# Kernel tuning notes

Hardware: AMD Instinct MI355X
Metric: run time of the kernel (lower is better)

## Reference

```python
import jax, jax.numpy as jnp
import numpy as np

# dims per init_kwargs
B, T, N = 2, 16, 8192
F0, F1, F2 = 4, 8, 8
K = 3
D0, D1 = 8, 4


def setup_inputs() -> dict:
    ks = jax.random.split(jax.random.key(0), 11)
    x = jax.random.normal(ks[0], (B, T, F0, N), jnp.float32)
    # GSO: random symmetric-ish shift operator, scaled for spectral stability
    S = jax.random.normal(ks[1], (N, N), jnp.float32) / np.float32(np.sqrt(N))
    h1 = jax.random.normal(ks[2], (F1, K, F0), jnp.float32) * 0.1   # layer-1 filter taps
    b1 = jax.random.normal(ks[3], (F1, 1), jnp.float32) * 0.1
    h2 = jax.random.normal(ks[4], (F2, K, F1), jnp.float32) * 0.1   # layer-2 filter taps
    b2 = jax.random.normal(ks[5], (F2, 1), jnp.float32) * 0.1
    W1 = jax.random.normal(ks[6], (D0, F2), jnp.float32) * 0.1      # readout Linear 1
    bw1 = jax.random.normal(ks[7], (D0,), jnp.float32) * 0.1
    W2 = jax.random.normal(ks[8], (D1, D0), jnp.float32) * 0.1      # readout Linear 2
    bw2 = jax.random.normal(ks[9], (D1,), jnp.float32) * 0.1
    return {"x": x, "S": S, "h1": h1, "b1": b1, "h2": h2, "b2": b2,
            "W1": W1, "bw1": bw1, "W2": W2, "bw2": bw2}


def graph_filter(x, S, h, b):
    # x: [B,T,Fin,N]; h: [Fout,K,Fin]; b: [Fout,1]
    # z_k = z_{k-1} @ S  (diffusion over node dim, LSIGF with E=1, no delay)
    taps = [x]
    for _ in range(h.shape[1] - 1):
        taps.append(jnp.matmul(taps[-1], S))
    z = jnp.stack(taps, axis=2)                       # [B,T,K,Fin,N]
    return jnp.einsum('gkf,btkfn->btgn', h, z) + b    # [B,T,Fout,N]


def reference(x, S, h1, b1, h2, b2, W1, bw1, W2, bw2):
    y = jnp.tanh(graph_filter(x, S, h1, b1))          # [B,T,F1,N]
    y = jnp.tanh(graph_filter(y, S, h2, b2))          # [B,T,F2,N]
    # per-node readout: Linear over feature axis
    y = jnp.swapaxes(y, 2, 3)                         # [B,T,N,F2]
    y = jnp.tanh(jnp.einsum('btnf,df->btnd', y, W1) + bw1)
    y = jnp.einsum('btnd,ed->btne', y, W2) + bw2
    return jnp.swapaxes(y, 2, 3)                      # [B,T,D1,N]
```

## Files before the change

### kernel.cpp

```cpp
#include <hip/hip_runtime.h>
#include <math.h>

constexpr int NN = 8192;

typedef short bh8 __attribute__((ext_vector_type(8)));
typedef float fl4 __attribute__((ext_vector_type(4)));

__device__ __forceinline__ float bf2f(ushort h) {
  return __uint_as_float(((uint)h) << 16);
}
__device__ __forceinline__ ushort f2bf(float f) {
  uint u = __float_as_uint(f);
  return (ushort)((u + 0x7fffu + ((u >> 16) & 1u)) >> 16);
}

constexpr size_t OFF_P  = 16;
constexpr size_t OFF_XC = 4096;
constexpr size_t OFF_Z1 = OFF_XC + 2097152;
constexpr size_t OFF_Y1 = OFF_Z1 + 2097152;
constexpr size_t OFF_V1 = OFF_Y1 + 4194304;
constexpr size_t OFF_ST = 33554432;
constexpr size_t OFF_CF = 167772160;

constexpr int PO_H1 = 0, PO_B1 = 96, PO_H2 = 104, PO_B2 = 296;
constexpr int PO_W1 = 304, PO_BW1 = 368, PO_W2 = 376, PO_BW2 = 408;

__global__ __launch_bounds__(256) void detect_convert(
    const ushort* __restrict__ Sraw,
    const void* h1, const void* b1, const void* h2, const void* b2,
    const void* W1, const void* bw1, const void* W2, const void* bw2,
    char* __restrict__ ws) {
  __shared__ int smax[256];
  __shared__ int sflag;
  const int t = threadIdx.x;
  int mx = 0;
  for (int k = 0; k < 32; ++k) {
    ushort u = Sraw[(size_t)(t * 32 + k) * 2];
    int e = (u >> 7) & 0xff;
    mx = mx > e ? mx : e;
  }
  smax[t] = mx;
  __syncthreads();
  for (int s = 128; s > 0; s >>= 1) {
    if (t < s) smax[t] = smax[t] > smax[t + s] ? smax[t] : smax[t + s];
    __syncthreads();
  }
  if (t == 0) {
    sflag = (smax[0] >= 0x90) ? 1 : 0;
    *(int*)ws = sflag;
  }
  __syncthreads();
  const int f32 = sflag;
  float* pb = (float*)(ws + OFF_P);
  const void* ptrs[8] = {h1, b1, h2, b2, W1, bw1, W2, bw2};
  const int offs[8] = {PO_H1, PO_B1, PO_H2, PO_B2, PO_W1, PO_BW1, PO_W2, PO_BW2};
  const int lens[8] = {96, 8, 192, 8, 64, 8, 32, 4};
  for (int idx = t; idx < 412; idx += 256) {
#pragma unroll
    for (int s = 0; s < 8; ++s) {
      if (idx >= offs[s] && idx < offs[s] + lens[s]) {
        const int j = idx - offs[s];
        pb[idx] = f32 ? ((const float*)ptrs[s])[j]
                      : bf2f(((const ushort*)ptrs[s])[j]);
      }
    }
  }
}

__global__ __launch_bounds__(256) void convert_x(const void* __restrict__ xraw,
                                                 const char* __restrict__ wsro,
                                                 ushort* __restrict__ xc) {
  const int f32 = *(const int*)wsro;
  const int i = (blockIdx.x * 256 + threadIdx.x) * 4;
  if (f32) {
    float4 v = *(const float4*)((const float*)xraw + i);
    uint2 o;
    o.x = (uint)f2bf(v.x) | ((uint)f2bf(v.y) << 16);
    o.y = (uint)f2bf(v.z) | ((uint)f2bf(v.w) << 16);
    *(uint2*)&xc[i] = o;
  } else {
    *(uint2*)&xc[i] = *(const uint2*)((const ushort*)xraw + i);
  }
}

template <int Z>
__global__ __launch_bounds__(256) void reduce_cvt(const float* __restrict__ src,
                                                  size_t slice,
                                                  ushort* __restrict__ dst) {
  const size_t i = (size_t)(blockIdx.x * 256 + threadIdx.x) * 4;
  float4 s = *(const float4*)&src[i];
#pragma unroll
  for (int z = 1; z < Z; ++z) {
    float4 t = *(const float4*)&src[(size_t)z * slice + i];
    s.x += t.x; s.y += t.y; s.z += t.z; s.w += t.w;
  }
  uint2 o;
  o.x = (uint)f2bf(s.x) | ((uint)f2bf(s.y) << 16);
  o.y = (uint)f2bf(s.z) | ((uint)f2bf(s.w) << 16);
  *(uint2*)&dst[i] = o;
}

__global__ __launch_bounds__(256) void transpose_k(const ushort* __restrict__ Sraw,
                                                   const char* __restrict__ wsro,
                                                   ushort* __restrict__ St) {
  __shared__ uint tileU[64][33];
  const int f32 = *(const int*)wsro;
  const int t = threadIdx.x;
  const int tn = blockIdx.x * 64;
  const int tk = blockIdx.y * 64;
  {
    const int kp = t >> 3;
    const int c  = (t & 7) * 8;
    if (f32) {
      const float* r0 = (const float*)Sraw + (size_t)(tk + 2 * kp) * NN + tn + c;
      float4 a0 = *(const float4*)r0;
      float4 a1 = *(const float4*)(r0 + 4);
      float4 b0 = *(const float4*)(r0 + NN);
      float4 b1 = *(const float4*)(r0 + NN + 4);
      tileU[c + 0][kp] = (uint)f2bf(a0.x) | ((uint)f2bf(b0.x) << 16);
      tileU[c + 1][kp] = (uint)f2bf(a0.y) | ((uint)f2bf(b0.y) << 16);
      tileU[c + 2][kp] = (uint)f2bf(a0.z) | ((uint)f2bf(b0.z) << 16);
      tileU[c + 3][kp] = (uint)f2bf(a0.w) | ((uint)f2bf(b0.w) << 16);
      tileU[c + 4][kp] = (uint)f2bf(a1.x) | ((uint)f2bf(b1.x) << 16);
      tileU[c + 5][kp] = (uint)f2bf(a1.y) | ((uint)f2bf(b1.y) << 16);
      tileU[c + 6][kp] = (uint)f2bf(a1.z) | ((uint)f2bf(b1.z) << 16);
      tileU[c + 7][kp] = (uint)f2bf(a1.w) | ((uint)f2bf(b1.w) << 16);
    } else {
      const ushort* r0 = Sraw + (size_t)(tk + 2 * kp) * NN + tn + c;
      uint4 ua = *(const uint4*)r0;
      uint4 ub = *(const uint4*)(r0 + NN);
      const ushort* ap = (const ushort*)&ua;
      const ushort* bp = (const ushort*)&ub;
#pragma unroll
      for (int j = 0; j < 8; ++j)
        tileU[c + j][kp] = (uint)ap[j] | ((uint)bp[j] << 16);
    }
  }
  __syncthreads();
  {
    const int n = t >> 2;
#pragma unroll
    for (int it = 0; it < 2; ++it) {
      const int q = (t & 3) + 4 * it;
      uint4 w;
      w.x = tileU[n][q * 4 + 0];
      w.y = tileU[n][q * 4 + 1];
      w.z = tileU[n][q * 4 + 2];
      w.w = tileU[n][q * 4 + 3];
      *(uint4*)&St[(size_t)(tn + n) * NN + tk + q * 8] = w;
    }
  }
}

template <int KR>
__global__ __launch_bounds__(256, 2) void gemm_t(const ushort* __restrict__ A,
                                                 const ushort* __restrict__ St,
                                                 float* __restrict__ CF) {
  __shared__ ushort As[2][128 * 64];
  __shared__ ushort Bs[2][128 * 64];
  const int tid = threadIdx.x;
  const int wave = tid >> 6, lane = tid & 63;
  const int lrow = lane & 15, quad = lane >> 4;
  const int m0 = blockIdx.y * 128;
  const int n0 = blockIdx.x * 128;
  const int kc0 = blockIdx.z * KR;
  const int wm = (wave & 1) * 64;
  const int wn = (wave >> 1) * 64;
  float* CP = CF + (size_t)blockIdx.z * (size_t)(gridDim.y * 128) * NN;

  const ushort* ap[4];
  const ushort* bp[4];
#pragma unroll
  for (int r = 0; r < 4; ++r) {
    const int s = r * 256 + tid;
    const int row = s >> 3, g = (s & 7) ^ (row & 7);
    ap[r] = A + (size_t)(m0 + row) * NN + g * 8;
    bp[r] = St + (size_t)(n0 + row) * NN + g * 8;
  }

  fl4 acc[4][4];
#pragma unroll
  for (int i = 0; i < 4; ++i)
#pragma unroll
    for (int j = 0; j < 4; ++j) acc[i][j] = (fl4){0.f, 0.f, 0.f, 0.f};

#define STAGE(buf, kc)                                                         \
  {                                                                            \
    _Pragma("unroll")                                                          \
    for (int r = 0; r < 4; ++r) {                                              \
      __builtin_amdgcn_global_load_lds(                                        \
          (__attribute__((address_space(1))) void*)(ap[r] + (kc)),             \
          (__attribute__((address_space(3))) void*)                            \
              &As[buf][(r * 256 + wave * 64) * 8],                             \
          16, 0, 0);                                                           \
      __builtin_amdgcn_global_load_lds(                                        \
          (__attribute__((address_space(1))) void*)(bp[r] + (kc)),             \
          (__attribute__((address_space(3))) void*)                            \
              &Bs[buf][(r * 256 + wave * 64) * 8],                             \
          16, 0, 0);                                                           \
    }                                                                          \
  }

#define COMPUTE(buf)                                                           \
  {                                                                            \
    _Pragma("unroll")                                                          \
    for (int is = 0; is < 2; ++is) {                                           \
      bh8 af[4], bf[4];                                                        \
      const int G = is * 4 + quad;                                             \
      _Pragma("unroll")                                                        \
      for (int i = 0; i < 4; ++i) {                                            \
        const int row = wm + i * 16 + lrow;                                    \
        af[i] = *(const bh8*)&As[buf][row * 64 + ((G ^ (row & 7)) * 8)];       \
      }                                                                        \
      _Pragma("unroll")                                                        \
      for (int j = 0; j < 4; ++j) {                                            \
        const int row = wn + j * 16 + lrow;                                    \
        bf[j] = *(const bh8*)&Bs[buf][row * 64 + ((G ^ (row & 7)) * 8)];       \
      }                                                                        \
      _Pragma("unroll")                                                        \
      for (int i = 0; i < 4; ++i)                                              \
        _Pragma("unroll")                                                      \
        for (int j = 0; j < 4; ++j)                                            \
          acc[i][j] = __builtin_amdgcn_mfma_f32_16x16x32_bf16(af[i], bf[j],    \
                                                              acc[i][j], 0, 0, 0); \
    }                                                                          \
  }

#define BARRIER()                                                              \
  {                                                                            \
    asm volatile("" ::: "memory");                                             \
    __builtin_amdgcn_s_barrier();                                              \
    asm volatile("" ::: "memory");                                             \
  }

  STAGE(0, kc0)
  STAGE(1, kc0 + 64)
  const int kend = kc0 + KR;
#pragma unroll 1
  for (int kc = kc0; kc < kend; kc += 128) {
    asm volatile("s_waitcnt vmcnt(8)" ::: "memory");
    BARRIER()
    COMPUTE(0)
    asm volatile("s_waitcnt lgkmcnt(0)" ::: "memory");
    BARRIER()
    if (kc + 128 < kend) {
      STAGE(0, kc + 128)
      asm volatile("s_waitcnt vmcnt(8)" ::: "memory");
    } else {
      asm volatile("s_waitcnt vmcnt(0)" ::: "memory");
    }
    BARRIER()
    COMPUTE(1)
    if (kc + 192 < kend) {
      asm volatile("s_waitcnt lgkmcnt(0)" ::: "memory");
      BARRIER()
      STAGE(1, kc + 192)
    }
  }
#undef STAGE
#undef COMPUTE
#undef BARRIER

#pragma unroll
  for (int i = 0; i < 4; ++i)
#pragma unroll
    for (int j = 0; j < 4; ++j)
#pragma unroll
      for (int rr = 0; rr < 4; ++rr) {
        const int row = m0 + wm + i * 16 + quad * 4 + rr;
        const int col = n0 + wn + j * 16 + lrow;
        CP[(size_t)row * NN + col] = acc[i][j][rr];
      }
}

__global__ __launch_bounds__(256) void combine1(const ushort* __restrict__ xc,
                                                const ushort* __restrict__ z1,
                                                const float* __restrict__ z2f,
                                                const char* __restrict__ wsro,
                                                ushort* __restrict__ y1) {
  const float* pb = (const float*)(wsro + OFF_P);
  __shared__ float hs[96], bs[8];
  const int t = threadIdx.x;
  if (t < 96) hs[t] = pb[PO_H1 + t];
  if (t < 8) bs[t] = pb[PO_B1 + t];
  __syncthreads();
  const int idx = blockIdx.x * 256 + t;
  const int bt = idx >> 11;
  const int n4 = (idx & 2047) * 4;
  float acc[8][4];
#pragma unroll
  for (int g = 0; g < 8; ++g)
#pragma unroll
    for (int v = 0; v < 4; ++v) acc[g][v] = bs[g];
#pragma unroll
  for (int k = 0; k < 3; ++k)
#pragma unroll
    for (int f = 0; f < 4; ++f) {
      const size_t off = (size_t)(bt * 4 + f) * NN + n4;
      float val[4];
      if (k == 2) {
        float4 w = *(const float4*)&z2f[off];
#pragma unroll
        for (int z = 1; z < 8; ++z) {
          float4 u = *(const float4*)&z2f[(size_t)z * 1048576 + off];
          w.x += u.x; w.y += u.y; w.z += u.z; w.w += u.w;
        }
        val[0] = w.x; val[1] = w.y; val[2] = w.z; val[3] = w.w;
      } else {
        const ushort* pp = (k == 0) ? xc : z1;
        uint2 w = *(const uint2*)&pp[off];
        val[0] = bf2f(w.x & 0xffff); val[1] = bf2f(w.x >> 16);
        val[2] = bf2f(w.y & 0xffff); val[3] = bf2f(w.y >> 16);
      }
#pragma unroll
      for (int g = 0; g < 8; ++g) {
        const float hw = hs[(g * 3 + k) * 4 + f];
#pragma unroll
        for (int v = 0; v < 4; ++v) acc[g][v] += hw * val[v];
      }
    }
#pragma unroll
  for (int g = 0; g < 8; ++g) {
    ushort o[4];
#pragma unroll
    for (int v = 0; v < 4; ++v) o[v] = f2bf(tanhf(acc[g][v]));
    uint2 w;
    w.x = (uint)o[0] | ((uint)o[1] << 16);
    w.y = (uint)o[2] | ((uint)o[3] << 16);
    *(uint2*)&y1[(size_t)(bt * 8 + g) * NN + n4] = w;
  }
}

__global__ __launch_bounds__(256) void combine2(const ushort* __restrict__ y1,
                                                const ushort* __restrict__ v1,
                                                const float* __restrict__ v2f,
                                                const char* __restrict__ wsro,
                                                void* __restrict__ outv) {
  const float* pb = (const float*)(wsro + OFF_P);
  const int f32 = *(const int*)wsro;
  __shared__ float h2s[192], W1s[64], W2s[32], b2s[8], bw1s[8], bw2s[4];
  const int t = threadIdx.x;
  if (t < 192) h2s[t] = pb[PO_H2 + t];
  if (t < 64) W1s[t] = pb[PO_W1 + t];
  if (t < 32) W2s[t] = pb[PO_W2 + t];
  if (t < 8) { b2s[t] = pb[PO_B2 + t]; bw1s[t] = pb[PO_BW1 + t]; }
  if (t < 4) bw2s[t] = pb[PO_BW2 + t];
  __syncthreads();
  const int idx = blockIdx.x * 256 + t;
  const int bt = idx >> 12;
  const int n2 = (idx & 4095) * 2;
  float acc[8][2];
#pragma unroll
  for (int g = 0; g < 8; ++g) { acc[g][0] = b2s[g]; acc[g][1] = b2s[g]; }
#pragma unroll
  for (int k = 0; k < 3; ++k)
#pragma unroll
    for (int g1 = 0; g1 < 8; ++g1) {
      const size_t off = (size_t)(bt * 8 + g1) * NN + n2;
      float v0, v1v;
      if (k == 2) {
        float2 w = *(const float2*)&v2f[off];
#pragma unroll
        for (int z = 1; z < 4; ++z) {
          float2 u = *(const float2*)&v2f[(size_t)z * 2097152 + off];
          w.x += u.x; w.y += u.y;
        }
        v0 = w.x; v1v = w.y;
      } else {
        const ushort* pp = (k == 0) ? y1 : v1;
        uint w = *(const uint*)&pp[off];
        v0 = bf2f(w & 0xffff); v1v = bf2f(w >> 16);
      }
#pragma unroll
      for (int g2 = 0; g2 < 8; ++g2) {
        const float hw = h2s[(g2 * 3 + k) * 8 + g1];
        acc[g2][0] += hw * v0;
        acc[g2][1] += hw * v1v;
      }
    }
#pragma unroll
  for (int g = 0; g < 8; ++g) {
    acc[g][0] = tanhf(acc[g][0]);
    acc[g][1] = tanhf(acc[g][1]);
  }
  float o[4][2];
#pragma unroll
  for (int e = 0; e < 4; ++e) { o[e][0] = bw2s[e]; o[e][1] = bw2s[e]; }
#pragma unroll
  for (int d = 0; d < 8; ++d) {
    float s0 = bw1s[d], s1 = bw1s[d];
#pragma unroll
    for (int f = 0; f < 8; ++f) {
      const float w = W1s[d * 8 + f];
      s0 += w * acc[f][0];
      s1 += w * acc[f][1];
    }
    s0 = tanhf(s0);
    s1 = tanhf(s1);
#pragma unroll
    for (int e = 0; e < 4; ++e) {
      const float w = W2s[e * 8 + d];
      o[e][0] += w * s0;
      o[e][1] += w * s1;
    }
  }
#pragma unroll
  for (int e = 0; e < 4; ++e) {
    const size_t off = (size_t)(bt * 4 + e) * NN + n2;
    if (f32) {
      float2 w = {o[e][0], o[e][1]};
      *(float2*)&((float*)outv)[off] = w;
    } else {
      uint w = (uint)f2bf(o[e][0]) | ((uint)f2bf(o[e][1]) << 16);
      *(uint*)&((ushort*)outv)[off] = w;
    }
  }
}

extern "C" void kernel_launch(void* const* d_in, const int* in_sizes, int n_in,
                              void* d_out, int out_size, void* d_ws,
                              size_t ws_size, hipStream_t stream) {
  (void)in_sizes; (void)n_in; (void)out_size; (void)ws_size;
  const void* x = d_in[0];
  const ushort* S = (const ushort*)d_in[1];
  char* ws = (char*)d_ws;
  ushort* xc = (ushort*)(ws + OFF_XC);
  ushort* z1 = (ushort*)(ws + OFF_Z1);
  ushort* y1 = (ushort*)(ws + OFF_Y1);
  ushort* v1 = (ushort*)(ws + OFF_V1);
  float* CF = (float*)(ws + OFF_CF);
  ushort* St = (ushort*)(ws + OFF_ST);

  detect_convert<<<1, 256, 0, stream>>>(S, d_in[2], d_in[3], d_in[4], d_in[5],
                                        d_in[6], d_in[7], d_in[8], d_in[9], ws);
  convert_x<<<1024, 256, 0, stream>>>(x, ws, xc);
  transpose_k<<<dim3(128, 128), 256, 0, stream>>>(S, ws, St);

  gemm_t<1024><<<dim3(64, 1, 8), 256, 0, stream>>>(xc, St, CF);
  reduce_cvt<8><<<1024, 256, 0, stream>>>(CF, (size_t)1048576, z1);

  gemm_t<1024><<<dim3(64, 1, 8), 256, 0, stream>>>(z1, St, CF);
  combine1<<<256, 256, 0, stream>>>(xc, z1, CF, ws, y1);

  gemm_t<2048><<<dim3(64, 2, 4), 256, 0, stream>>>(y1, St, CF);
  reduce_cvt<4><<<2048, 256, 0, stream>>>(CF, (size_t)2097152, v1);

  gemm_t<2048><<<dim3(64, 2, 4), 256, 0, stream>>>(v1, St, CF);
  combine2<<<512, 256, 0, stream>>>(y1, v1, CF, ws, (void*)d_out);
}
```

Measured before the change: 591.3 us.

## Fuse all stages into one persistent kernel with software grid barriers

Replaces the sequence of ten kernel launches (convert, transpose, four split-K GEMMs, reductions and combines) with a single persistent kernel of 512 blocks that runs every stage in order, separated by atomic-counter grid barriers. This is meant to remove launch gaps and kernel-boundary drains between the short stages. The cost is that the transpose is now a grid-stride loop over fewer blocks, and progress depends on all 512 blocks being co-resident (two per CU), with a spin barrier that has a timeout guard and could silently break synchronisation.

```diff
diff --git a/kernel.cpp b/kernel.cpp
--- a/kernel.cpp
+++ b/kernel.cpp
@@ -2,6 +2,7 @@
 #include <math.h>
 
 constexpr int NN = 8192;
+constexpr int NBLK = 512;
 
 typedef short bh8 __attribute__((ext_vector_type(8)));
 typedef float fl4 __attribute__((ext_vector_type(4)));
@@ -14,18 +15,19 @@
   return (ushort)((u + 0x7fffu + ((u >> 16) & 1u)) >> 16);
 }
 
-constexpr size_t OFF_P  = 16;
-constexpr size_t OFF_XC = 4096;
-constexpr size_t OFF_Z1 = OFF_XC + 2097152;
-constexpr size_t OFF_Y1 = OFF_Z1 + 2097152;
-constexpr size_t OFF_V1 = OFF_Y1 + 4194304;
-constexpr size_t OFF_ST = 33554432;
-constexpr size_t OFF_CF = 167772160;
+constexpr size_t OFF_P   = 16;
+constexpr size_t OFF_BAR = 2048;
+constexpr size_t OFF_XC  = 4096;
+constexpr size_t OFF_Z1  = OFF_XC + 2097152;
+constexpr size_t OFF_Y1  = OFF_Z1 + 2097152;
+constexpr size_t OFF_V1  = OFF_Y1 + 4194304;
+constexpr size_t OFF_ST  = 33554432;
+constexpr size_t OFF_CF  = 167772160;
 
 constexpr int PO_H1 = 0, PO_B1 = 96, PO_H2 = 104, PO_B2 = 296;
 constexpr int PO_W1 = 304, PO_BW1 = 368, PO_W2 = 376, PO_BW2 = 408;
 
-__global__ __launch_bounds__(256) void detect_convert(
+__global__ __launch_bounds__(256) void pre_kernel(
     const ushort* __restrict__ Sraw,
     const void* h1, const void* b1, const void* h2, const void* b2,
     const void* W1, const void* bw1, const void* W2, const void* bw2,
@@ -48,6 +50,7 @@
   if (t == 0) {
     sflag = (smax[0] >= 0x90) ? 1 : 0;
     *(int*)ws = sflag;
+    *(int*)(ws + OFF_BAR) = 0;
   }
   __syncthreads();
   const int f32 = sflag;
@@ -67,106 +70,33 @@
   }
 }
 
-__global__ __launch_bounds__(256) void convert_x(const void* __restrict__ xraw,
-                                                 const char* __restrict__ wsro,
-                                                 ushort* __restrict__ xc) {
-  const int f32 = *(const int*)wsro;
-  const int i = (blockIdx.x * 256 + threadIdx.x) * 4;
-  if (f32) {
-    float4 v = *(const float4*)((const float*)xraw + i);
-    uint2 o;
-    o.x = (uint)f2bf(v.x) | ((uint)f2bf(v.y) << 16);
-    o.y = (uint)f2bf(v.z) | ((uint)f2bf(v.w) << 16);
-    *(uint2*)&xc[i] = o;
-  } else {
-    *(uint2*)&xc[i] = *(const uint2*)((const ushort*)xraw + i);
-  }
-}
-
-template <int Z>
-__global__ __launch_bounds__(256) void reduce_cvt(const float* __restrict__ src,
-                                                  size_t slice,
-                                                  ushort* __restrict__ dst) {
-  const size_t i = (size_t)(blockIdx.x * 256 + threadIdx.x) * 4;
-  float4 s = *(const float4*)&src[i];
-#pragma unroll
-  for (int z = 1; z < Z; ++z) {
-    float4 t = *(const float4*)&src[(size_t)z * slice + i];
-    s.x += t.x; s.y += t.y; s.z += t.z; s.w += t.w;
-  }
-  uint2 o;
-  o.x = (uint)f2bf(s.x) | ((uint)f2bf(s.y) << 16);
-  o.y = (uint)f2bf(s.z) | ((uint)f2bf(s.w) << 16);
-  *(uint2*)&dst[i] = o;
-}
-
-__global__ __launch_bounds__(256) void transpose_k(const ushort* __restrict__ Sraw,
-                                                   const char* __restrict__ wsro,
-                                                   ushort* __restrict__ St) {
-  __shared__ uint tileU[64][33];
-  const int f32 = *(const int*)wsro;
-  const int t = threadIdx.x;
-  const int tn = blockIdx.x * 64;
-  const int tk = blockIdx.y * 64;
-  {
-    const int kp = t >> 3;
-    const int c  = (t & 7) * 8;
-    if (f32) {
-      const float* r0 = (const float*)Sraw + (size_t)(tk + 2 * kp) * NN + tn + c;
-      float4 a0 = *(const float4*)r0;
-      float4 a1 = *(const float4*)(r0 + 4);
-      float4 b0 = *(const float4*)(r0 + NN);
-      float4 b1 = *(const float4*)(r0 + NN + 4);
-      tileU[c + 0][kp] = (uint)f2bf(a0.x) | ((uint)f2bf(b0.x) << 16);
-      tileU[c + 1][kp] = (uint)f2bf(a0.y) | ((uint)f2bf(b0.y) << 16);
-      tileU[c + 2][kp] = (uint)f2bf(a0.z) | ((uint)f2bf(b0.z) << 16);
-      tileU[c + 3][kp] = (uint)f2bf(a0.w) | ((uint)f2bf(b0.w) << 16);
-      tileU[c + 4][kp] = (uint)f2bf(a1.x) | ((uint)f2bf(b1.x) << 16);
-      tileU[c + 5][kp] = (uint)f2bf(a1.y) | ((uint)f2bf(b1.y) << 16);
-      tileU[c + 6][kp] = (uint)f2bf(a1.z) | ((uint)f2bf(b1.z) << 16);
-      tileU[c + 7][kp] = (uint)f2bf(a1.w) | ((uint)f2bf(b1.w) << 16);
-    } else {
-      const ushort* r0 = Sraw + (size_t)(tk + 2 * kp) * NN + tn + c;
-      uint4 ua = *(const uint4*)r0;
-      uint4 ub = *(const uint4*)(r0 + NN);
-      const ushort* ap = (const ushort*)&ua;
-      const ushort* bp = (const ushort*)&ub;
-#pragma unroll
-      for (int j = 0; j < 8; ++j)
-        tileU[c + j][kp] = (uint)ap[j] | ((uint)bp[j] << 16);
-    }
-  }
+__device__ __forceinline__ void gridbar(int* cnt, int phase) {
   __syncthreads();
-  {
-    const int n = t >> 2;
-#pragma unroll
-    for (int it = 0; it < 2; ++it) {
-      const int q = (t & 3) + 4 * it;
-      uint4 w;
-      w.x = tileU[n][q * 4 + 0];
-      w.y = tileU[n][q * 4 + 1];
-      w.z = tileU[n][q * 4 + 2];
-      w.w = tileU[n][q * 4 + 3];
-      *(uint4*)&St[(size_t)(tn + n) * NN + tk + q * 8] = w;
-    }
-  }
-}
-
-template <int KR>
-__global__ __launch_bounds__(256, 2) void gemm_t(const ushort* __restrict__ A,
-                                                 const ushort* __restrict__ St,
-                                                 float* __restrict__ CF) {
-  __shared__ ushort As[2][128 * 64];
-  __shared__ ushort Bs[2][128 * 64];
+  if (threadIdx.x == 0) {
+    __threadfence();
+    __hip_atomic_fetch_add(cnt, 1, __ATOMIC_RELEASE, __HIP_MEMORY_SCOPE_AGENT);
+    const int target = phase * NBLK;
+    int guard = 0;
+    while (__hip_atomic_load(cnt, __ATOMIC_ACQUIRE, __HIP_MEMORY_SCOPE_AGENT) <
+           target) {
+      __builtin_amdgcn_s_sleep(8);
+      if (++guard > (1 << 20)) break;
+    }
+    __threadfence();
+  }
+  __syncthreads();
+}
+
+__device__ __forceinline__ void gemm_stage(const ushort* __restrict__ A,
+                                           const ushort* __restrict__ St,
+                                           float* __restrict__ CP,
+                                           int m0, int n0, int kc0, int KR,
+                                           ushort* sh) {
   const int tid = threadIdx.x;
   const int wave = tid >> 6, lane = tid & 63;
   const int lrow = lane & 15, quad = lane >> 4;
-  const int m0 = blockIdx.y * 128;
-  const int n0 = blockIdx.x * 128;
-  const int kc0 = blockIdx.z * KR;
   const int wm = (wave & 1) * 64;
   const int wn = (wave >> 1) * 64;
-  float* CP = CF + (size_t)blockIdx.z * (size_t)(gridDim.y * 128) * NN;
 
   const ushort* ap[4];
   const ushort* bp[4];
@@ -191,12 +121,12 @@
       __builtin_amdgcn_global_load_lds(                                        \
           (__attribute__((address_space(1))) void*)(ap[r] + (kc)),             \
           (__attribute__((address_space(3))) void*)                            \
-              &As[buf][(r * 256 + wave * 64) * 8],                             \
+              &sh[(buf) * 8192 + (r * 256 + wave * 64) * 8],                   \
           16, 0, 0);                                                           \
       __builtin_amdgcn_global_load_lds(                                        \
           (__attribute__((address_space(1))) void*)(bp[r] + (kc)),             \
           (__attribute__((address_space(3))) void*)                            \
-              &Bs[buf][(r * 256 + wave * 64) * 8],                             \
+              &sh[16384 + (buf) * 8192 + (r * 256 + wave * 64) * 8],           \
           16, 0, 0);                                                           \
     }                                                                          \
   }
@@ -210,12 +140,14 @@
       _Pragma("unroll")                                                        \
       for (int i = 0; i < 4; ++i) {                                            \
         const int row = wm + i * 16 + lrow;                                    \
-        af[i] = *(const bh8*)&As[buf][row * 64 + ((G ^ (row & 7)) * 8)];       \
+        af[i] = *(const bh8*)&sh[(buf) * 8192 + row * 64 +                     \
+                                 ((G ^ (row & 7)) * 8)];                       \
       }                                                                        \
       _Pragma("unroll")                                                        \
       for (int j = 0; j < 4; ++j) {                                            \
         const int row = wn + j * 16 + lrow;                                    \
-        bf[j] = *(const bh8*)&Bs[buf][row * 64 + ((G ^ (row & 7)) * 8)];       \
+        bf[j] = *(const bh8*)&sh[16384 + (buf) * 8192 + row * 64 +             \
+                                 ((G ^ (row & 7)) * 8)];                       \
       }                                                                        \
       _Pragma("unroll")                                                        \
       for (int i = 0; i < 4; ++i)                                              \
@@ -226,7 +158,7 @@
     }                                                                          \
   }
 
-#define BARRIER()                                                              \
+#define BBAR()                                                                 \
   {                                                                            \
     asm volatile("" ::: "memory");                                             \
     __builtin_amdgcn_s_barrier();                                              \
@@ -239,27 +171,27 @@
 #pragma unroll 1
   for (int kc = kc0; kc < kend; kc += 128) {
     asm volatile("s_waitcnt vmcnt(8)" ::: "memory");
-    BARRIER()
+    BBAR()
     COMPUTE(0)
     asm volatile("s_waitcnt lgkmcnt(0)" ::: "memory");
-    BARRIER()
+    BBAR()
     if (kc + 128 < kend) {
       STAGE(0, kc + 128)
       asm volatile("s_waitcnt vmcnt(8)" ::: "memory");
     } else {
       asm volatile("s_waitcnt vmcnt(0)" ::: "memory");
     }
-    BARRIER()
+    BBAR()
     COMPUTE(1)
     if (kc + 192 < kend) {
       asm volatile("s_waitcnt lgkmcnt(0)" ::: "memory");
-      BARRIER()
+      BBAR()
       STAGE(1, kc + 192)
     }
   }
 #undef STAGE
 #undef COMPUTE
-#undef BARRIER
+#undef BBAR
 
 #pragma unroll
   for (int i = 0; i < 4; ++i)
@@ -273,146 +205,269 @@
       }
 }
 
-__global__ __launch_bounds__(256) void combine1(const ushort* __restrict__ xc,
-                                                const ushort* __restrict__ z1,
-                                                const float* __restrict__ z2f,
-                                                const char* __restrict__ wsro,
-                                                ushort* __restrict__ y1) {
-  const float* pb = (const float*)(wsro + OFF_P);
-  __shared__ float hs[96], bs[8];
+__global__ __launch_bounds__(256, 2) void mono(const void* __restrict__ xraw,
+                                               const ushort* __restrict__ Sraw,
+                                               char* __restrict__ ws,
+                                               void* __restrict__ outv) {
+  __shared__ ushort shg[4][8192];
+  ushort* sh = &shg[0][0];
   const int t = threadIdx.x;
-  if (t < 96) hs[t] = pb[PO_H1 + t];
-  if (t < 8) bs[t] = pb[PO_B1 + t];
-  __syncthreads();
-  const int idx = blockIdx.x * 256 + t;
-  const int bt = idx >> 11;
-  const int n4 = (idx & 2047) * 4;
-  float acc[8][4];
-#pragma unroll
-  for (int g = 0; g < 8; ++g)
-#pragma unroll
-    for (int v = 0; v < 4; ++v) acc[g][v] = bs[g];
-#pragma unroll
-  for (int k = 0; k < 3; ++k)
-#pragma unroll
-    for (int f = 0; f < 4; ++f) {
-      const size_t off = (size_t)(bt * 4 + f) * NN + n4;
-      float val[4];
-      if (k == 2) {
-        float4 w = *(const float4*)&z2f[off];
-#pragma unroll
-        for (int z = 1; z < 8; ++z) {
-          float4 u = *(const float4*)&z2f[(size_t)z * 1048576 + off];
-          w.x += u.x; w.y += u.y; w.z += u.z; w.w += u.w;
-        }
-        val[0] = w.x; val[1] = w.y; val[2] = w.z; val[3] = w.w;
+  const int bid = blockIdx.x;
+  const int f32 = *(const int*)ws;
+  int* cnt = (int*)(ws + OFF_BAR);
+  const float* pb = (const float*)(ws + OFF_P);
+  ushort* xc = (ushort*)(ws + OFF_XC);
+  ushort* z1 = (ushort*)(ws + OFF_Z1);
+  ushort* y1 = (ushort*)(ws + OFF_Y1);
+  ushort* v1 = (ushort*)(ws + OFF_V1);
+  float* CF = (float*)(ws + OFF_CF);
+  ushort* St = (ushort*)(ws + OFF_ST);
+
+#pragma unroll 1
+  for (int it = 0; it < 2; ++it) {
+    const int i = (it * 131072 + bid * 256 + t) * 4;
+    if (f32) {
+      float4 v = *(const float4*)((const float*)xraw + i);
+      uint2 o;
+      o.x = (uint)f2bf(v.x) | ((uint)f2bf(v.y) << 16);
+      o.y = (uint)f2bf(v.z) | ((uint)f2bf(v.w) << 16);
+      *(uint2*)&xc[i] = o;
+    } else {
+      *(uint2*)&xc[i] = *(const uint2*)((const ushort*)xraw + i);
+    }
+  }
+
+  {
+    uint(*tileU)[33] = (uint(*)[33])sh;
+#pragma unroll 1
+    for (int tt = bid; tt < 16384; tt += NBLK) {
+      const int tn = (tt & 127) * 64;
+      const int tk = (tt >> 7) * 64;
+      __syncthreads();
+      {
+        const int kp = t >> 3;
+        const int c = (t & 7) * 8;
+        if (f32) {
+          const float* r0 =
+              (const float*)Sraw + (size_t)(tk + 2 * kp) * NN + tn + c;
+          float4 a0 = *(const float4*)r0;
+          float4 a1 = *(const float4*)(r0 + 4);
+          float4 b0 = *(const float4*)(r0 + NN);
+          float4 b1 = *(const float4*)(r0 + NN + 4);
+          tileU[c + 0][kp] = (uint)f2bf(a0.x) | ((uint)f2bf(b0.x) << 16);
+          tileU[c + 1][kp] = (uint)f2bf(a0.y) | ((uint)f2bf(b0.y) << 16);
+          tileU[c + 2][kp] = (uint)f2bf(a0.z) | ((uint)f2bf(b0.z) << 16);
+          tileU[c + 3][kp] = (uint)f2bf(a0.w) | ((uint)f2bf(b0.w) << 16);
+          tileU[c + 4][kp] = (uint)f2bf(a1.x) | ((uint)f2bf(b1.x) << 16);
+          tileU[c + 5][kp] = (uint)f2bf(a1.y) | ((uint)f2bf(b1.y) << 16);
+          tileU[c + 6][kp] = (uint)f2bf(a1.z) | ((uint)f2bf(b1.z) << 16);
+          tileU[c + 7][kp] = (uint)f2bf(a1.w) | ((uint)f2bf(b1.w) << 16);
+        } else {
+          const ushort* r0 = Sraw + (size_t)(tk + 2 * kp) * NN + tn + c;
+          uint4 ua = *(const uint4*)r0;
+          uint4 ub = *(const uint4*)(r0 + NN);
+          const ushort* apx = (const ushort*)&ua;
+          const ushort* bpx = (const ushort*)&ub;
+#pragma unroll
+          for (int j = 0; j < 8; ++j)
+            tileU[c + j][kp] = (uint)apx[j] | ((uint)bpx[j] << 16);
+        }
+      }
+      __syncthreads();
+      {
+        const int n = t >> 2;
+#pragma unroll
+        for (int it = 0; it < 2; ++it) {
+          const int q = (t & 3) + 4 * it;
+          uint4 w;
+          w.x = tileU[n][q * 4 + 0];
+          w.y = tileU[n][q * 4 + 1];
+          w.z = tileU[n][q * 4 + 2];
+          w.w = tileU[n][q * 4 + 3];
+          *(uint4*)&St[(size_t)(tn + n) * NN + tk + q * 8] = w;
+        }
+      }
+    }
+  }
+
+  gridbar(cnt, 1);
+
+  gemm_stage(xc, St, CF + (size_t)(bid >> 6) * 1048576, 0, (bid & 63) * 128,
+             (bid >> 6) * 1024, 1024, sh);
+  gridbar(cnt, 2);
+
+#pragma unroll 1
+  for (int it = 0; it < 2; ++it) {
+    const size_t i = (size_t)(it * 131072 + bid * 256 + t) * 4;
+    float4 s = *(const float4*)&CF[i];
+#pragma unroll
+    for (int z = 1; z < 8; ++z) {
+      float4 u = *(const float4*)&CF[(size_t)z * 1048576 + i];
+      s.x += u.x; s.y += u.y; s.z += u.z; s.w += u.w;
+    }
+    uint2 o;
+    o.x = (uint)f2bf(s.x) | ((uint)f2bf(s.y) << 16);
+    o.y = (uint)f2bf(s.z) | ((uint)f2bf(s.w) << 16);
+    *(uint2*)&z1[i] = o;
+  }
+  gridbar(cnt, 3);
+
+  gemm_stage(z1, St, CF + (size_t)(bid >> 6) * 1048576, 0, (bid & 63) * 128,
+             (bid >> 6) * 1024, 1024, sh);
+  gridbar(cnt, 4);
+
+  {
+    float* hs = (float*)sh;
+    float* bs = hs + 96;
+    if (t < 96) hs[t] = pb[PO_H1 + t];
+    if (t < 8) bs[t] = pb[PO_B1 + t];
+    __syncthreads();
+    const int idx = bid * 256 + t;
+    const int bt = idx >> 12;
+    const int n2 = (idx & 4095) * 2;
+    float acc[8][2];
+#pragma unroll
+    for (int g = 0; g < 8; ++g) { acc[g][0] = bs[g]; acc[g][1] = bs[g]; }
+#pragma unroll
+    for (int k = 0; k < 3; ++k)
+#pragma unroll
+      for (int f = 0; f < 4; ++f) {
+        const size_t off = (size_t)(bt * 4 + f) * NN + n2;
+        float v0, v1v;
+        if (k == 2) {
+          float2 w = *(const float2*)&CF[off];
+#pragma unroll
+          for (int z = 1; z < 8; ++z) {
+            float2 u = *(const float2*)&CF[(size_t)z * 1048576 + off];
+            w.x += u.x; w.y += u.y;
+          }
+          v0 = w.x; v1v = w.y;
+        } else {
+          const ushort* pp = (k == 0) ? xc : z1;
+          uint w = *(const uint*)&pp[off];
+          v0 = bf2f(w & 0xffff); v1v = bf2f(w >> 16);
+        }
+#pragma unroll
+        for (int g = 0; g < 8; ++g) {
+          const float hw = hs[(g * 3 + k) * 4 + f];
+          acc[g][0] += hw * v0;
+          acc[g][1] += hw * v1v;
+        }
+      }
+#pragma unroll
+    for (int g = 0; g < 8; ++g) {
+      uint w = (uint)f2bf(tanhf(acc[g][0])) |
+               ((uint)f2bf(tanhf(acc[g][1])) << 16);
+      *(uint*)&y1[(size_t)(bt * 8 + g) * NN + n2] = w;
+    }
+  }
+  gridbar(cnt, 5);
+
+  gemm_stage(y1, St, CF + (size_t)(bid >> 7) * 2097152, ((bid >> 6) & 1) * 128,
+             (bid & 63) * 128, (bid >> 7) * 2048, 2048, sh);
+  gridbar(cnt, 6);
+
+#pragma unroll 1
+  for (int it = 0; it < 4; ++it) {
+    const size_t i = (size_t)(it * 131072 + bid * 256 + t) * 4;
+    float4 s = *(const float4*)&CF[i];
+#pragma unroll
+    for (int z = 1; z < 4; ++z) {
+      float4 u = *(const float4*)&CF[(size_t)z * 2097152 + i];
+      s.x += u.x; s.y += u.y; s.z += u.z; s.w += u.w;
+    }
+    uint2 o;
+    o.x = (uint)f2bf(s.x) | ((uint)f2bf(s.y) << 16);
+    o.y = (uint)f2bf(s.z) | ((uint)f2bf(s.w) << 16);
+    *(uint2*)&v1[i] = o;
+  }
+  gridbar(cnt, 7);
+
+  gemm_stage(v1, St, CF + (size_t)(bid >> 7) * 2097152, ((bid >> 6) & 1) * 128,
+             (bid & 63) * 128, (bid >> 7) * 2048, 2048, sh);
+  gridbar(cnt, 8);
+
+  {
+    float* h2s = (float*)sh;
+    float* W1s = h2s + 192;
+    float* W2s = W1s + 64;
+    float* b2s = W2s + 32;
+    float* bw1s = b2s + 8;
+    float* bw2s = bw1s + 8;
+    if (t < 192) h2s[t] = pb[PO_H2 + t];
+    if (t < 64) W1s[t] = pb[PO_W1 + t];
+    if (t < 32) W2s[t] = pb[PO_W2 + t];
+    if (t < 8) { b2s[t] = pb[PO_B2 + t]; bw1s[t] = pb[PO_BW1 + t]; }
+    if (t < 4) bw2s[t] = pb[PO_BW2 + t];
+    __syncthreads();
+    const int idx = bid * 256 + t;
+    const int bt = idx >> 12;
+    const int n2 = (idx & 4095) * 2;
+    float acc[8][2];
+#pragma unroll
+    for (int g = 0; g < 8; ++g) { acc[g][0] = b2s[g]; acc[g][1] = b2s[g]; }
+#pragma unroll
+    for (int k = 0; k < 3; ++k)
+#pragma unroll
+      for (int g1 = 0; g1 < 8; ++g1) {
+        const size_t off = (size_t)(bt * 8 + g1) * NN + n2;
+        float v0, v1v;
+        if (k == 2) {
+          float2 w = *(const float2*)&CF[off];
+#pragma unroll
+          for (int z = 1; z < 4; ++z) {
+            float2 u = *(const float2*)&CF[(size_t)z * 2097152 + off];
+            w.x += u.x; w.y += u.y;
+          }
+          v0 = w.x; v1v = w.y;
+        } else {
+          const ushort* pp = (k == 0) ? y1 : v1;
+          uint w = *(const uint*)&pp[off];
+          v0 = bf2f(w & 0xffff); v1v = bf2f(w >> 16);
+        }
+#pragma unroll
+        for (int g2 = 0; g2 < 8; ++g2) {
+          const float hw = h2s[(g2 * 3 + k) * 8 + g1];
+          acc[g2][0] += hw * v0;
+          acc[g2][1] += hw * v1v;
+        }
+      }
+#pragma unroll
+    for (int g = 0; g < 8; ++g) {
+      acc[g][0] = tanhf(acc[g][0]);
+      acc[g][1] = tanhf(acc[g][1]);
+    }
+    float o[4][2];
+#pragma unroll
+    for (int e = 0; e < 4; ++e) { o[e][0] = bw2s[e]; o[e][1] = bw2s[e]; }
+#pragma unroll
+    for (int d = 0; d < 8; ++d) {
+      float s0 = bw1s[d], s1 = bw1s[d];
+#pragma unroll
+      for (int f = 0; f < 8; ++f) {
+        const float w = W1s[d * 8 + f];
+        s0 += w * acc[f][0];
+        s1 += w * acc[f][1];
+      }
+      s0 = tanhf(s0);
+      s1 = tanhf(s1);
+#pragma unroll
+      for (int e = 0; e < 4; ++e) {
+        const float w = W2s[e * 8 + d];
+        o[e][0] += w * s0;
+        o[e][1] += w * s1;
+      }
+    }
+#pragma unroll
+    for (int e = 0; e < 4; ++e) {
+      const size_t off = (size_t)(bt * 4 + e) * NN + n2;
+      if (f32) {
+        float2 w = {o[e][0], o[e][1]};
+        *(float2*)&((float*)outv)[off] = w;
       } else {
-        const ushort* pp = (k == 0) ? xc : z1;
-        uint2 w = *(const uint2*)&pp[off];
-        val[0] = bf2f(w.x & 0xffff); val[1] = bf2f(w.x >> 16);
-        val[2] = bf2f(w.y & 0xffff); val[3] = bf2f(w.y >> 16);
-      }
-#pragma unroll
-      for (int g = 0; g < 8; ++g) {
-        const float hw = hs[(g * 3 + k) * 4 + f];
-#pragma unroll
-        for (int v = 0; v < 4; ++v) acc[g][v] += hw * val[v];
-      }
-    }
-#pragma unroll
-  for (int g = 0; g < 8; ++g) {
-    ushort o[4];
-#pragma unroll
-    for (int v = 0; v < 4; ++v) o[v] = f2bf(tanhf(acc[g][v]));
-    uint2 w;
-    w.x = (uint)o[0] | ((uint)o[1] << 16);
-    w.y = (uint)o[2] | ((uint)o[3] << 16);
-    *(uint2*)&y1[(size_t)(bt * 8 + g) * NN + n4] = w;
-  }
-}
-
-__global__ __launch_bounds__(256) void combine2(const ushort* __restrict__ y1,
-                                                const ushort* __restrict__ v1,
-                                                const float* __restrict__ v2f,
-                                                const char* __restrict__ wsro,
-                                                void* __restrict__ outv) {
-  const float* pb = (const float*)(wsro + OFF_P);
-  const int f32 = *(const int*)wsro;
-  __shared__ float h2s[192], W1s[64], W2s[32], b2s[8], bw1s[8], bw2s[4];
-  const int t = threadIdx.x;
-  if (t < 192) h2s[t] = pb[PO_H2 + t];
-  if (t < 64) W1s[t] = pb[PO_W1 + t];
-  if (t < 32) W2s[t] = pb[PO_W2 + t];
-  if (t < 8) { b2s[t] = pb[PO_B2 + t]; bw1s[t] = pb[PO_BW1 + t]; }
-  if (t < 4) bw2s[t] = pb[PO_BW2 + t];
-  __syncthreads();
-  const int idx = blockIdx.x * 256 + t;
-  const int bt = idx >> 12;
-  const int n2 = (idx & 4095) * 2;
-  float acc[8][2];
-#pragma unroll
-  for (int g = 0; g < 8; ++g) { acc[g][0] = b2s[g]; acc[g][1] = b2s[g]; }
-#pragma unroll
-  for (int k = 0; k < 3; ++k)
-#pragma unroll
-    for (int g1 = 0; g1 < 8; ++g1) {
-      const size_t off = (size_t)(bt * 8 + g1) * NN + n2;
-      float v0, v1v;
-      if (k == 2) {
-        float2 w = *(const float2*)&v2f[off];
-#pragma unroll
-        for (int z = 1; z < 4; ++z) {
-          float2 u = *(const float2*)&v2f[(size_t)z * 2097152 + off];
-          w.x += u.x; w.y += u.y;
-        }
-        v0 = w.x; v1v = w.y;
-      } else {
-        const ushort* pp = (k == 0) ? y1 : v1;
-        uint w = *(const uint*)&pp[off];
-        v0 = bf2f(w & 0xffff); v1v = bf2f(w >> 16);
-      }
-#pragma unroll
-      for (int g2 = 0; g2 < 8; ++g2) {
-        const float hw = h2s[(g2 * 3 + k) * 8 + g1];
-        acc[g2][0] += hw * v0;
-        acc[g2][1] += hw * v1v;
-      }
-    }
-#pragma unroll
-  for (int g = 0; g < 8; ++g) {
-    acc[g][0] = tanhf(acc[g][0]);
-    acc[g][1] = tanhf(acc[g][1]);
-  }
-  float o[4][2];
-#pragma unroll
-  for (int e = 0; e < 4; ++e) { o[e][0] = bw2s[e]; o[e][1] = bw2s[e]; }
-#pragma unroll
-  for (int d = 0; d < 8; ++d) {
-    float s0 = bw1s[d], s1 = bw1s[d];
-#pragma unroll
-    for (int f = 0; f < 8; ++f) {
-      const float w = W1s[d * 8 + f];
-      s0 += w * acc[f][0];
-      s1 += w * acc[f][1];
-    }
-    s0 = tanhf(s0);
-    s1 = tanhf(s1);
-#pragma unroll
-    for (int e = 0; e < 4; ++e) {
-      const float w = W2s[e * 8 + d];
-      o[e][0] += w * s0;
-      o[e][1] += w * s1;
-    }
-  }
-#pragma unroll
-  for (int e = 0; e < 4; ++e) {
-    const size_t off = (size_t)(bt * 4 + e) * NN + n2;
-    if (f32) {
-      float2 w = {o[e][0], o[e][1]};
-      *(float2*)&((float*)outv)[off] = w;
-    } else {
-      uint w = (uint)f2bf(o[e][0]) | ((uint)f2bf(o[e][1]) << 16);
-      *(uint*)&((ushort*)outv)[off] = w;
+        uint w = (uint)f2bf(o[e][0]) | ((uint)f2bf(o[e][1]) << 16);
+        *(uint*)&((ushort*)outv)[off] = w;
+      }
     }
   }
 }
@@ -424,27 +479,8 @@
   const void* x = d_in[0];
   const ushort* S = (const ushort*)d_in[1];
   char* ws = (char*)d_ws;
-  ushort* xc = (ushort*)(ws + OFF_XC);
-  ushort* z1 = (ushort*)(ws + OFF_Z1);
-  ushort* y1 = (ushort*)(ws + OFF_Y1);
-  ushort* v1 = (ushort*)(ws + OFF_V1);
-  float* CF = (float*)(ws + OFF_CF);
-  ushort* St = (ushort*)(ws + OFF_ST);
-
-  detect_convert<<<1, 256, 0, stream>>>(S, d_in[2], d_in[3], d_in[4], d_in[5],
-                                        d_in[6], d_in[7], d_in[8], d_in[9], ws);
-  convert_x<<<1024, 256, 0, stream>>>(x, ws, xc);
-  transpose_k<<<dim3(128, 128), 256, 0, stream>>>(S, ws, St);
-
-  gemm_t<1024><<<dim3(64, 1, 8), 256, 0, stream>>>(xc, St, CF);
-  reduce_cvt<8><<<1024, 256, 0, stream>>>(CF, (size_t)1048576, z1);
-
-  gemm_t<1024><<<dim3(64, 1, 8), 256, 0, stream>>>(z1, St, CF);
-  combine1<<<256, 256, 0, stream>>>(xc, z1, CF, ws, y1);
-
-  gemm_t<2048><<<dim3(64, 2, 4), 256, 0, stream>>>(y1, St, CF);
-  reduce_cvt<4><<<2048, 256, 0, stream>>>(CF, (size_t)2097152, v1);
-
-  gemm_t<2048><<<dim3(64, 2, 4), 256, 0, stream>>>(v1, St, CF);
-  combine2<<<512, 256, 0, stream>>>(y1, v1, CF, ws, (void*)d_out);
-}
+
+  pre_kernel<<<1, 256, 0, stream>>>(S, d_in[2], d_in[3], d_in[4], d_in[5],
+                                    d_in[6], d_in[7], d_in[8], d_in[9], ws);
+  mono<<<NBLK, 256, 0, stream>>>(x, S, ws, (void*)d_out);
+}
```

Measured after the change: 1.349 ms. +128.1%, slower.

## Fuse split-K reduction and combine epilogues into GEMM via last-block tickets

Applied to the files above, without the earlier changes.

Each split-K GEMM now increments a per-tile atomic ticket, and the last-arriving block sums the partial slices and writes the reduced output directly. For the second GEMM it also applies the layer-1 filter combine with tanh. This removes the separate reduce_cvt and combine1 launches. The x conversion is folded into the transpose kernel and the tickets are zeroed in the pre-kernel. The cost is that the reduction runs serially in one block per tile, plus added atomics and fences.

```diff
diff --git a/kernel.cpp b/kernel.cpp
--- a/kernel.cpp
+++ b/kernel.cpp
@@ -15,17 +15,19 @@
 }
 
 constexpr size_t OFF_P  = 16;
+constexpr size_t OFF_TK = 2048;
 constexpr size_t OFF_XC = 4096;
 constexpr size_t OFF_Z1 = OFF_XC + 2097152;
 constexpr size_t OFF_Y1 = OFF_Z1 + 2097152;
 constexpr size_t OFF_V1 = OFF_Y1 + 4194304;
 constexpr size_t OFF_ST = 33554432;
 constexpr size_t OFF_CF = 167772160;
+constexpr size_t OFF_V2 = 201326592;
 
 constexpr int PO_H1 = 0, PO_B1 = 96, PO_H2 = 104, PO_B2 = 296;
 constexpr int PO_W1 = 304, PO_BW1 = 368, PO_W2 = 376, PO_BW2 = 408;
 
-__global__ __launch_bounds__(256) void detect_convert(
+__global__ __launch_bounds__(256) void pre_kernel(
     const ushort* __restrict__ Sraw,
     const void* h1, const void* b1, const void* h2, const void* b2,
     const void* W1, const void* bw1, const void* W2, const void* bw2,
@@ -50,6 +52,9 @@
     *(int*)ws = sflag;
   }
   __syncthreads();
+  int* tk = (int*)(ws + OFF_TK);
+  tk[t] = 0;
+  tk[256 + t] = 0;
   const int f32 = sflag;
   float* pb = (float*)(ws + OFF_P);
   const void* ptrs[8] = {h1, b1, h2, b2, W1, bw1, W2, bw2};
@@ -67,45 +72,26 @@
   }
 }
 
-__global__ __launch_bounds__(256) void convert_x(const void* __restrict__ xraw,
-                                                 const char* __restrict__ wsro,
-                                                 ushort* __restrict__ xc) {
-  const int f32 = *(const int*)wsro;
-  const int i = (blockIdx.x * 256 + threadIdx.x) * 4;
-  if (f32) {
-    float4 v = *(const float4*)((const float*)xraw + i);
-    uint2 o;
-    o.x = (uint)f2bf(v.x) | ((uint)f2bf(v.y) << 16);
-    o.y = (uint)f2bf(v.z) | ((uint)f2bf(v.w) << 16);
-    *(uint2*)&xc[i] = o;
-  } else {
-    *(uint2*)&xc[i] = *(const uint2*)((const ushort*)xraw + i);
-  }
-}
-
-template <int Z>
-__global__ __launch_bounds__(256) void reduce_cvt(const float* __restrict__ src,
-                                                  size_t slice,
-                                                  ushort* __restrict__ dst) {
-  const size_t i = (size_t)(blockIdx.x * 256 + threadIdx.x) * 4;
-  float4 s = *(const float4*)&src[i];
-#pragma unroll
-  for (int z = 1; z < Z; ++z) {
-    float4 t = *(const float4*)&src[(size_t)z * slice + i];
-    s.x += t.x; s.y += t.y; s.z += t.z; s.w += t.w;
-  }
-  uint2 o;
-  o.x = (uint)f2bf(s.x) | ((uint)f2bf(s.y) << 16);
-  o.y = (uint)f2bf(s.z) | ((uint)f2bf(s.w) << 16);
-  *(uint2*)&dst[i] = o;
-}
-
-__global__ __launch_bounds__(256) void transpose_k(const ushort* __restrict__ Sraw,
-                                                   const char* __restrict__ wsro,
-                                                   ushort* __restrict__ St) {
+__global__ __launch_bounds__(256) void transpose_cvt(
+    const ushort* __restrict__ Sraw, const void* __restrict__ xraw,
+    const char* __restrict__ wsro, ushort* __restrict__ St,
+    ushort* __restrict__ xc) {
   __shared__ uint tileU[64][33];
   const int f32 = *(const int*)wsro;
   const int t = threadIdx.x;
+  const int bid = blockIdx.y * gridDim.x + blockIdx.x;
+  if (bid < 1024) {
+    const int i = (bid * 256 + t) * 4;
+    if (f32) {
+      float4 v = *(const float4*)((const float*)xraw + i);
+      uint2 o;
+      o.x = (uint)f2bf(v.x) | ((uint)f2bf(v.y) << 16);
+      o.y = (uint)f2bf(v.z) | ((uint)f2bf(v.w) << 16);
+      *(uint2*)&xc[i] = o;
+    } else {
+      *(uint2*)&xc[i] = *(const uint2*)((const ushort*)xraw + i);
+    }
+  }
   const int tn = blockIdx.x * 64;
   const int tk = blockIdx.y * 64;
   {
@@ -152,12 +138,15 @@
   }
 }
 
-template <int KR>
-__global__ __launch_bounds__(256, 2) void gemm_t(const ushort* __restrict__ A,
-                                                 const ushort* __restrict__ St,
-                                                 float* __restrict__ CF) {
-  __shared__ ushort As[2][128 * 64];
-  __shared__ ushort Bs[2][128 * 64];
+template <int KR, int Z, int MODE>
+__global__ __launch_bounds__(256, 2) void gemm_t(
+    const ushort* __restrict__ A, const ushort* __restrict__ St,
+    float* __restrict__ CF, void* __restrict__ OUT,
+    const ushort* __restrict__ T0, const ushort* __restrict__ T1,
+    char* __restrict__ ws, int tkBase) {
+  __shared__ ushort sh[32768];
+  __shared__ float prm[104];
+  __shared__ int lastFlag;
   const int tid = threadIdx.x;
   const int wave = tid >> 6, lane = tid & 63;
   const int lrow = lane & 15, quad = lane >> 4;
@@ -191,12 +180,12 @@
       __builtin_amdgcn_global_load_lds(                                        \
           (__attribute__((address_space(1))) void*)(ap[r] + (kc)),             \
           (__attribute__((address_space(3))) void*)                            \
-              &As[buf][(r * 256 + wave * 64) * 8],                             \
+              &sh[(buf) * 8192 + (r * 256 + wave * 64) * 8],                   \
           16, 0, 0);                                                           \
       __builtin_amdgcn_global_load_lds(                                        \
           (__attribute__((address_space(1))) void*)(bp[r] + (kc)),             \
           (__attribute__((address_space(3))) void*)                            \
-              &Bs[buf][(r * 256 + wave * 64) * 8],                             \
+              &sh[16384 + (buf) * 8192 + (r * 256 + wave * 64) * 8],           \
           16, 0, 0);                                                           \
     }                                                                          \
   }
@@ -210,12 +199,14 @@
       _Pragma("unroll")                                                        \
       for (int i = 0; i < 4; ++i) {                                            \
         const int row = wm + i * 16 + lrow;                                    \
-        af[i] = *(const bh8*)&As[buf][row * 64 + ((G ^ (row & 7)) * 8)];       \
+        af[i] = *(const bh8*)&sh[(buf) * 8192 + row * 64 +                     \
+                                 ((G ^ (row & 7)) * 8)];                       \
       }                                                                        \
       _Pragma("unroll")                                                        \
       for (int j = 0; j < 4; ++j) {                                            \
         const int row = wn + j * 16 + lrow;                                    \
-        bf[j] = *(const bh8*)&Bs[buf][row * 64 + ((G ^ (row & 7)) * 8)];       \
+        bf[j] = *(const bh8*)&sh[16384 + (buf) * 8192 + row * 64 +             \
+                                 ((G ^ (row & 7)) * 8)];                       \
       }                                                                        \
       _Pragma("unroll")                                                        \
       for (int i = 0; i < 4; ++i)                                              \
@@ -226,7 +217,7 @@
     }                                                                          \
   }
 
-#define BARRIER()                                                              \
+#define BBAR()                                                                 \
   {                                                                            \
     asm volatile("" ::: "memory");                                             \
     __builtin_amdgcn_s_barrier();                                              \
@@ -239,27 +230,27 @@
 #pragma unroll 1
   for (int kc = kc0; kc < kend; kc += 128) {
     asm volatile("s_waitcnt vmcnt(8)" ::: "memory");
-    BARRIER()
+    BBAR()
     COMPUTE(0)
     asm volatile("s_waitcnt lgkmcnt(0)" ::: "memory");
-    BARRIER()
+    BBAR()
     if (kc + 128 < kend) {
       STAGE(0, kc + 128)
       asm volatile("s_waitcnt vmcnt(8)" ::: "memory");
     } else {
       asm volatile("s_waitcnt vmcnt(0)" ::: "memory");
     }
-    BARRIER()
+    BBAR()
     COMPUTE(1)
     if (kc + 192 < kend) {
       asm volatile("s_waitcnt lgkmcnt(0)" ::: "memory");
-      BARRIER()
+      BBAR()
       STAGE(1, kc + 192)
     }
   }
 #undef STAGE
 #undef COMPUTE
-#undef BARRIER
+#undef BBAR
 
 #pragma unroll
   for (int i = 0; i < 4; ++i)
@@ -271,63 +262,96 @@
         const int col = n0 + wn + j * 16 + lrow;
         CP[(size_t)row * NN + col] = acc[i][j][rr];
       }
-}
-
-__global__ __launch_bounds__(256) void combine1(const ushort* __restrict__ xc,
-                                                const ushort* __restrict__ z1,
-                                                const float* __restrict__ z2f,
-                                                const char* __restrict__ wsro,
-                                                ushort* __restrict__ y1) {
-  const float* pb = (const float*)(wsro + OFF_P);
-  __shared__ float hs[96], bs[8];
-  const int t = threadIdx.x;
-  if (t < 96) hs[t] = pb[PO_H1 + t];
-  if (t < 8) bs[t] = pb[PO_B1 + t];
-  __syncthreads();
-  const int idx = blockIdx.x * 256 + t;
-  const int bt = idx >> 11;
-  const int n4 = (idx & 2047) * 4;
-  float acc[8][4];
-#pragma unroll
-  for (int g = 0; g < 8; ++g)
-#pragma unroll
-    for (int v = 0; v < 4; ++v) acc[g][v] = bs[g];
-#pragma unroll
-  for (int k = 0; k < 3; ++k)
-#pragma unroll
-    for (int f = 0; f < 4; ++f) {
-      const size_t off = (size_t)(bt * 4 + f) * NN + n4;
-      float val[4];
-      if (k == 2) {
-        float4 w = *(const float4*)&z2f[off];
-#pragma unroll
-        for (int z = 1; z < 8; ++z) {
-          float4 u = *(const float4*)&z2f[(size_t)z * 1048576 + off];
-          w.x += u.x; w.y += u.y; w.z += u.z; w.w += u.w;
+
+  __syncthreads();
+  const int tileId = blockIdx.y * gridDim.x + blockIdx.x;
+  int* ticket = (int*)(ws + OFF_TK) + tkBase + tileId;
+  if (tid == 0) {
+    __threadfence();
+    int old = __hip_atomic_fetch_add(ticket, 1, __ATOMIC_ACQ_REL,
+                                     __HIP_MEMORY_SCOPE_AGENT);
+    lastFlag = (old == Z - 1) ? 1 : 0;
+  }
+  __syncthreads();
+  if (!lastFlag) return;
+  __threadfence();
+
+  const size_t SLST = (size_t)gridDim.y * 128 * NN;
+  if constexpr (MODE == 2) {
+    float* zl = (float*)sh;
+    const float* pb = (const float*)(ws + OFF_P);
+    for (int e = tid; e < 4096; e += 256) {
+      const int row = e >> 5;
+      const int c = (e & 31) * 4;
+      const size_t base = (size_t)row * NN + n0 + c;
+      float4 s = *(const float4*)&CF[base];
+#pragma unroll
+      for (int z = 1; z < Z; ++z) {
+        float4 u = *(const float4*)&CF[(size_t)z * SLST + base];
+        s.x += u.x; s.y += u.y; s.z += u.z; s.w += u.w;
+      }
+      *(float4*)&zl[row * 128 + c] = s;
+    }
+    if (tid < 96) prm[tid] = pb[PO_H1 + tid];
+    if (tid < 8) prm[96 + tid] = pb[PO_B1 + tid];
+    __syncthreads();
+    ushort* y1o = (ushort*)OUT;
+    const int nl = (tid & 63) * 2;
+#pragma unroll 1
+    for (int p = 0; p < 8; ++p) {
+      const int bt = p * 4 + (tid >> 6);
+      float a2[8][2];
+#pragma unroll
+      for (int g = 0; g < 8; ++g) { a2[g][0] = prm[96 + g]; a2[g][1] = prm[96 + g]; }
+#pragma unroll
+      for (int k = 0; k < 3; ++k)
+#pragma unroll
+        for (int f = 0; f < 4; ++f) {
+          const int row = bt * 4 + f;
+          float v0, v1v;
+          if (k == 2) {
+            v0 = zl[row * 128 + nl];
+            v1v = zl[row * 128 + nl + 1];
+          } else {
+            const ushort* pp = (k == 0) ? T0 : T1;
+            uint w = *(const uint*)&pp[(size_t)row * NN + n0 + nl];
+            v0 = bf2f(w & 0xffff);
+            v1v = bf2f(w >> 16);
+          }
+#pragma unroll
+          for (int g = 0; g < 8; ++g) {
+            const float hw = prm[(g * 3 + k) * 4 + f];
+            a2[g][0] += hw * v0;
+            a2[g][1] += hw * v1v;
+          }
         }
-        val[0] = w.x; val[1] = w.y; val[2] = w.z; val[3] = w.w;
+#pragma unroll
+      for (int g = 0; g < 8; ++g) {
+        uint w = (uint)f2bf(tanhf(a2[g][0])) |
+                 ((uint)f2bf(tanhf(a2[g][1])) << 16);
+        *(uint*)&y1o[(size_t)(bt * 8 + g) * NN + n0 + nl] = w;
+      }
+    }
+  } else {
+    for (int e = tid; e < 4096; e += 256) {
+      const int row = e >> 5;
+      const int c = (e & 31) * 4;
+      const size_t base = (size_t)(m0 + row) * NN + n0 + c;
+      float4 s = *(const float4*)&CF[base];
+#pragma unroll
+      for (int z = 1; z < Z; ++z) {
+        float4 u = *(const float4*)&CF[(size_t)z * SLST + base];
+        s.x += u.x; s.y += u.y; s.z += u.z; s.w += u.w;
+      }
+      if constexpr (MODE == 0) {
+        uint2 o;
+        o.x = (uint)f2bf(s.x) | ((uint)f2bf(s.y) << 16);
+        o.y = (uint)f2bf(s.z) | ((uint)f2bf(s.w) << 16);
+        *(uint2*)&((ushort*)OUT)[base] = o;
       } else {
-        const ushort* pp = (k == 0) ? xc : z1;
-        uint2 w = *(const uint2*)&pp[off];
-        val[0] = bf2f(w.x & 0xffff); val[1] = bf2f(w.x >> 16);
-        val[2] = bf2f(w.y & 0xffff); val[3] = bf2f(w.y >> 16);
-      }
-#pragma unroll
-      for (int g = 0; g < 8; ++g) {
-        const float hw = hs[(g * 3 + k) * 4 + f];
-#pragma unroll
-        for (int v = 0; v < 4; ++v) acc[g][v] += hw * val[v];
-      }
-    }
-#pragma unroll
-  for (int g = 0; g < 8; ++g) {
-    ushort o[4];
-#pragma unroll
-    for (int v = 0; v < 4; ++v) o[v] = f2bf(tanhf(acc[g][v]));
-    uint2 w;
-    w.x = (uint)o[0] | ((uint)o[1] << 16);
-    w.y = (uint)o[2] | ((uint)o[3] << 16);
-    *(uint2*)&y1[(size_t)(bt * 8 + g) * NN + n4] = w;
+        *(float4*)&((float*)OUT)[base] = s;
+      }
+    }
   }
 }
 
@@ -360,11 +384,6 @@
       float v0, v1v;
       if (k == 2) {
         float2 w = *(const float2*)&v2f[off];
-#pragma unroll
-        for (int z = 1; z < 4; ++z) {
-          float2 u = *(const float2*)&v2f[(size_t)z * 2097152 + off];
-          w.x += u.x; w.y += u.y;
-        }
         v0 = w.x; v1v = w.y;
       } else {
         const ushort* pp = (k == 0) ? y1 : v1;
@@ -429,22 +448,20 @@
   ushort* y1 = (ushort*)(ws + OFF_Y1);
   ushort* v1 = (ushort*)(ws + OFF_V1);
   float* CF = (float*)(ws + OFF_CF);
+  float* v2 = (float*)(ws + OFF_V2);
   ushort* St = (ushort*)(ws + OFF_ST);
 
-  detect_convert<<<1, 256, 0, stream>>>(S, d_in[2], d_in[3], d_in[4], d_in[5],
-                                        d_in[6], d_in[7], d_in[8], d_in[9], ws);
-  convert_x<<<1024, 256, 0, stream>>>(x, ws, xc);
-  transpose_k<<<dim3(128, 128), 256, 0, stream>>>(S, ws, St);
-
-  gemm_t<1024><<<dim3(64, 1, 8), 256, 0, stream>>>(xc, St, CF);
-  reduce_cvt<8><<<1024, 256, 0, stream>>>(CF, (size_t)1048576, z1);
-
-  gemm_t<1024><<<dim3(64, 1, 8), 256, 0, stream>>>(z1, St, CF);
-  combine1<<<256, 256, 0, stream>>>(xc, z1, CF, ws, y1);
-
-  gemm_t<2048><<<dim3(64, 2, 4), 256, 0, stream>>>(y1, St, CF);
-  reduce_cvt<4><<<2048, 256, 0, stream>>>(CF, (size_t)2097152, v1);
-
-  gemm_t<2048><<<dim3(64, 2, 4), 256, 0, stream>>>(v1, St, CF);
-  combine2<<<512, 256, 0, stream>>>(y1, v1, CF, ws, (void*)d_out);
-}
+  pre_kernel<<<1, 256, 0, stream>>>(S, d_in[2], d_in[3], d_in[4], d_in[5],
+                                    d_in[6], d_in[7], d_in[8], d_in[9], ws);
+  transpose_cvt<<<dim3(128, 128), 256, 0, stream>>>(S, x, ws, St, xc);
+
+  gemm_t<1024, 8, 0><<<dim3(64, 1, 8), 256, 0, stream>>>(
+      xc, St, CF, (void*)z1, nullptr, nullptr, ws, 0);
+  gemm_t<1024, 8, 2><<<dim3(64, 1, 8), 256, 0, stream>>>(
+      z1, St, CF, (void*)y1, xc, z1, ws, 128);
+  gemm_t<2048, 4, 0><<<dim3(64, 2, 4), 256, 0, stream>>>(
+      y1, St, CF, (void*)v1, nullptr, nullptr, ws, 256);
+  gemm_t<2048, 4, 1><<<dim3(64, 2, 4), 256, 0, stream>>>(
+      v1, St, CF, (void*)v2, nullptr, nullptr, ws, 384);
+  combine2<<<512, 256, 0, stream>>>(y1, v1, v2, ws, (void*)d_out);
+}
```

Result: slower. 768.1 us (+29.9%).
